# Kernel tuning notes

Measured on AMD Instinct MI355X. Metric: run time of the kernel, lower is better.

## Reference

```python
import jax, jax.numpy as jnp
import numpy as np

B, N, DIM, H, DH, MLP, L = 4, 1024, 1024, 16, 64, 4096, 2
C = DIM // 4  # conditioning dim = 256


def setup_inputs() -> dict:
    key = jax.random.key(0)
    ks = jax.random.split(key, 12)
    s = 0.02
    return dict(
        x=jax.random.normal(ks[0], (B, N, DIM), jnp.float32),
        mu=jax.random.normal(ks[1], (B, N, C), jnp.float32),
        f=jax.random.normal(ks[2], (B, N, C), jnp.float32),
        Wqkv=jax.random.normal(ks[3], (L, DIM, 3 * H * DH), jnp.float32) * s,
        Wout=jax.random.normal(ks[4], (L, H * DH, DIM), jnp.float32) * s,
        bout=jnp.zeros((L, DIM), jnp.float32),
        W1=jax.random.normal(ks[5], (L, DIM, MLP), jnp.float32) * s,
        b1=jnp.zeros((L, MLP), jnp.float32),
        W2=jax.random.normal(ks[6], (L, MLP, DIM), jnp.float32) * s,
        b2=jnp.zeros((L, DIM), jnp.float32),
        Wmu=jax.random.normal(ks[7], (L, C, 6 * C), jnp.float32) * s,
        bmu=jnp.zeros((L, 6 * C), jnp.float32),
        Wf=jax.random.normal(ks[8], (L, C, 6 * 3 * C), jnp.float32) * s,
        bf=jnp.zeros((L, 6 * 3 * C), jnp.float32),
        g1=jnp.ones((L, DIM), jnp.float32),
        be1=jnp.zeros((L, DIM), jnp.float32),
        g2=jnp.ones((L, DIM), jnp.float32),
        be2=jnp.zeros((L, DIM), jnp.float32),
    )


def _ln(x, g, b):
    m = jnp.mean(x, -1, keepdims=True)
    v = jnp.mean((x - m) ** 2, -1, keepdims=True)
    return (x - m) * jax.lax.rsqrt(v + 1e-5) * g + b


def reference(x, mu, f, Wqkv, Wout, bout, W1, b1, W2, b2, Wmu, bmu, Wf, bf, g1, be1, g2, be2):
    scale = DH ** -0.5
    smu = jax.nn.silu(mu)  # SiLU applied to raw conditioning, shared across layers
    sf = jax.nn.silu(f)
    for i in range(L):
        mm = smu @ Wmu[i] + bmu[i]          # [B,N,6*C]
        mf = sf @ Wf[i] + bf[i]             # [B,N,6*3*C]
        mus = jnp.split(mm, 6, axis=-1)     # each [B,N,C]
        fs = jnp.split(mf, 6, axis=-1)      # each [B,N,3C]
        sh_a, sc_a, ga_a, sh_m, sc_m, ga_m = [
            jnp.concatenate([a, b_], -1) for a, b_ in zip(mus, fs)
        ]                                   # each [B,N,DIM]
        # attention branch
        h = _ln(x, g1[i], be1[i]) * (1 + sc_a) + sh_a
        qkv = h @ Wqkv[i]                   # [B,N,3*H*DH]
        q, k, v = [t.reshape(B, N, H, DH) for t in jnp.split(qkv, 3, axis=-1)]
        att = jax.nn.softmax(jnp.einsum('bihd,bjhd->bhij', q, k) * scale, axis=-1)
        o = jnp.einsum('bhij,bjhd->bihd', att, v).reshape(B, N, H * DH)
        x = x + ga_a * (o @ Wout[i] + bout[i])
        # MLP branch
        h2 = _ln(x, g2[i], be2[i]) * (1 + sc_m) + sh_m
        mlp = jax.nn.gelu(h2 @ W1[i] + b1[i], approximate=False) @ W2[i] + b2[i]
        x = x + ga_m * mlp
    return x
```

## Files before the change

### kernel.cpp

```cpp
#include <hip/hip_runtime.h>
#include <math.h>

#define BB 4
#define NN 1024
#define DIMD 1024
#define HHN 16
#define DHH 64
#define MLPD 4096
#define LLN 2
#define CCD 256
#define BNROWS (BB*NN)

typedef __attribute__((ext_vector_type(8))) _Float16 h8;
typedef __attribute__((ext_vector_type(4))) _Float16 h4;
typedef __attribute__((ext_vector_type(4))) float f32x4;

#define GLD16(gp, lp) __builtin_amdgcn_global_load_lds( \
    (const __attribute__((address_space(1))) void*)(gp), \
    (__attribute__((address_space(3))) void*)(lp), 16, 0, 0)

__global__ __launch_bounds__(256) void silu_kernel(const float* __restrict__ in,
                                                   _Float16* __restrict__ out, int n4) {
  int i = blockIdx.x * 256 + threadIdx.x;
  if (i < n4) {
    float4 v = ((const float4*)in)[i];
    h4 o;
    o[0] = (_Float16)(v.x / (1.f + __expf(-v.x)));
    o[1] = (_Float16)(v.y / (1.f + __expf(-v.y)));
    o[2] = (_Float16)(v.z / (1.f + __expf(-v.z)));
    o[3] = (_Float16)(v.w / (1.f + __expf(-v.w)));
    ((h4*)out)[i] = o;
  }
}

__global__ __launch_bounds__(256) void transpose_cast(const float* __restrict__ in,
                                                      _Float16* __restrict__ out,
                                                      int K, int N) {
  __shared__ float tile[64][68];
  int bx = blockIdx.x * 64;
  int by = blockIdx.y * 64;
  int tid = threadIdx.x;
  int r0 = tid >> 4, c4 = (tid & 15) * 4;
  #pragma unroll
  for (int i = 0; i < 4; i++) {
    float4 v = *(const float4*)(in + (size_t)(by + r0 + i * 16) * N + bx + c4);
    *(float4*)&tile[r0 + i * 16][c4] = v;
  }
  __syncthreads();
  #pragma unroll
  for (int i = 0; i < 4; i++) {
    int orow = r0 + i * 16;
    h4 o;
    #pragma unroll
    for (int j = 0; j < 4; j++) o[j] = (_Float16)tile[c4 + j][orow];
    *(h4*)(out + (size_t)(bx + orow) * K + by + c4) = o;
  }
}

__global__ __launch_bounds__(256) void v_transpose(const _Float16* __restrict__ qkv,
                                                   _Float16* __restrict__ vt) {
  __shared__ _Float16 t[64][72];
  int n0 = blockIdx.x * 64;
  int bh = blockIdx.y;
  int b = bh >> 4;
  const _Float16* src = qkv + (size_t)b * NN * 3072 + 2048 + (bh & 15) * 64;
  int tid = threadIdx.x;
  int row = tid >> 2, c0 = (tid & 3) * 16;
  *(h8*)&t[row][c0] = *(const h8*)(src + (size_t)(n0 + row) * 3072 + c0);
  *(h8*)&t[row][c0 + 8] = *(const h8*)(src + (size_t)(n0 + row) * 3072 + c0 + 8);
  __syncthreads();
  int d = tid >> 2, ns = (tid & 3) * 16;
  h8 o0, o1;
  #pragma unroll
  for (int j = 0; j < 8; j++) { o0[j] = t[ns + j][d]; o1[j] = t[ns + 8 + j][d]; }
  _Float16* dst = vt + ((size_t)bh * 64 + d) * NN + n0 + ns;
  *(h8*)dst = o0;
  *(h8*)(dst + 8) = o1;
}

template <int EPI, int BNT>
__global__ __launch_bounds__(256) void gemm_bt(
    const _Float16* __restrict__ A, const _Float16* __restrict__ Bt,
    int M, int Nt, int K,
    const float* __restrict__ bias,
    _Float16* __restrict__ outh,
    float* __restrict__ xio,
    const _Float16* __restrict__ mmb, const _Float16* __restrict__ mfb, int gchunk) {
  constexpr int NREP = BNT / 32;
  __shared__ _Float16 As[3][128 * 32];
  __shared__ _Float16 Bs[3][BNT * 32];
  const int tid = threadIdx.x;
  const int wave = tid >> 6, lane = tid & 63;
  const int brow = blockIdx.x * 128, bcol = blockIdx.y * BNT;
  const int wr = (wave >> 1) * 64, wc = (wave & 1) * (BNT / 2);
  const int r = lane & 15, g = lane >> 4;
  f32x4 acc[4][NREP];
  #pragma unroll
  for (int m = 0; m < 4; m++)
    #pragma unroll
    for (int n = 0; n < NREP; n++) acc[m][n] = (f32x4){0.f, 0.f, 0.f, 0.f};

  const int scol = ((lane & 3) ^ ((lane >> 3) & 3)) * 8;
  const _Float16* gA = A + (size_t)(brow + wave * 32 + (lane >> 2)) * K + scol;
  const _Float16* gB = Bt + (size_t)(bcol + wave * (BNT / 4) + (lane >> 2)) * K + scol;

  auto STAGE = [&](int slot, int k0) {
    GLD16(gA + k0, &As[slot][wave * 1024]);
    GLD16(gA + k0 + 16 * (size_t)K, &As[slot][wave * 1024 + 512]);
    if (BNT == 128) {
      GLD16(gB + k0, &Bs[slot][wave * 1024]);
      GLD16(gB + k0 + 16 * (size_t)K, &Bs[slot][wave * 1024 + 512]);
    } else {
      GLD16(gB + k0, &Bs[slot][wave * 512]);
    }
  };

  const int NT = K / 32;
  #pragma unroll
  for (int s = 0; s < 3; ++s)
    if (s < NT) STAGE(s, s * 32);

  const int gg = g ^ ((r >> 1) & 3);

  int cur = 0;
  for (int t = 0; t < NT; ++t) {
    const int rem = NT - 1 - t;
    if constexpr (BNT == 128) {
      if (rem >= 2)      asm volatile("s_waitcnt vmcnt(8)" ::: "memory");
      else if (rem == 1) asm volatile("s_waitcnt vmcnt(4)" ::: "memory");
      else               asm volatile("s_waitcnt vmcnt(0)" ::: "memory");
    } else {
      if (rem >= 2)      asm volatile("s_waitcnt vmcnt(6)" ::: "memory");
      else if (rem == 1) asm volatile("s_waitcnt vmcnt(3)" ::: "memory");
      else               asm volatile("s_waitcnt vmcnt(0)" ::: "memory");
    }
    __builtin_amdgcn_s_barrier();
    h8 af[4], bfr[NREP];
    #pragma unroll
    for (int m = 0; m < 4; m++) af[m] = *(const h8*)(&As[cur][(wr + m * 16 + r) * 32 + gg * 8]);
    #pragma unroll
    for (int n = 0; n < NREP; n++) bfr[n] = *(const h8*)(&Bs[cur][(wc + n * 16 + r) * 32 + gg * 8]);
    #pragma unroll
    for (int m = 0; m < 4; m++)
      #pragma unroll
      for (int n = 0; n < NREP; n++)
        acc[m][n] = __builtin_amdgcn_mfma_f32_16x16x32_f16(bfr[n], af[m], acc[m][n], 0, 0, 0);
    asm volatile("s_waitcnt lgkmcnt(0)" ::: "memory");
    __builtin_amdgcn_s_barrier();
    if (t + 3 < NT) STAGE(cur, (t + 3) * 32);
    cur = (cur == 2) ? 0 : cur + 1;
  }

  #pragma unroll
  for (int m = 0; m < 4; m++) {
    const int grow = brow + wr + m * 16 + r;
    #pragma unroll
    for (int n = 0; n < NREP; n++) {
      const int gcol = bcol + wc + n * 16 + 4 * g;
      float4 bv4 = bias ? *(const float4*)(bias + gcol) : float4{0.f, 0.f, 0.f, 0.f};
      float v[4] = {acc[m][n][0] + bv4.x, acc[m][n][1] + bv4.y,
                    acc[m][n][2] + bv4.z, acc[m][n][3] + bv4.w};
      if (EPI == 0) {
        h4 o;
        #pragma unroll
        for (int q = 0; q < 4; q++) o[q] = (_Float16)v[q];
        *(h4*)(outh + (size_t)grow * Nt + gcol) = o;
      } else if (EPI == 1) {
        h4 o;
        #pragma unroll
        for (int q = 0; q < 4; q++)
          o[q] = (_Float16)(0.5f * v[q] * (1.f + erff(v[q] * 0.70710678118f)));
        *(h4*)(outh + (size_t)grow * Nt + gcol) = o;
      } else {
        h4 gav = (gcol < CCD)
            ? *(const h4*)(mmb + (size_t)grow * (6 * CCD) + gchunk * CCD + gcol)
            : *(const h4*)(mfb + (size_t)grow * (18 * CCD) + gchunk * (3 * CCD) + (gcol - CCD));
        float4 xv = *(float4*)(xio + (size_t)grow * DIMD + gcol);
        xv.x += (float)gav[0] * v[0];
        xv.y += (float)gav[1] * v[1];
        xv.z += (float)gav[2] * v[2];
        xv.w += (float)gav[3] * v[3];
        *(float4*)(xio + (size_t)grow * DIMD + gcol) = xv;
      }
    }
  }
}

__global__ __launch_bounds__(256) void ln_mod(const float* __restrict__ x,
                                              const float* __restrict__ gam,
                                              const float* __restrict__ bet,
                                              const _Float16* __restrict__ mmb,
                                              const _Float16* __restrict__ mfb,
                                              int jsh, int jsc,
                                              _Float16* __restrict__ hout) {
  const int row = blockIdx.x;
  const int tid = threadIdx.x;
  const float* xr = x + (size_t)row * DIMD;
  float4 v = ((const float4*)xr)[tid];
  float s = v.x + v.y + v.z + v.w;
  float sq = v.x * v.x + v.y * v.y + v.z * v.z + v.w * v.w;
  #pragma unroll
  for (int off = 32; off > 0; off >>= 1) {
    s += __shfl_down(s, off);
    sq += __shfl_down(sq, off);
  }
  __shared__ float red[8];
  int wv = tid >> 6, ln = tid & 63;
  if (ln == 0) { red[wv] = s; red[4 + wv] = sq; }
  __syncthreads();
  s = red[0] + red[1] + red[2] + red[3];
  sq = red[4] + red[5] + red[6] + red[7];
  float mean = s * (1.f / DIMD);
  float var = sq * (1.f / DIMD) - mean * mean;
  float rs = rsqrtf(var + 1e-5f);
  int c0 = tid * 4;
  float4 gm = ((const float4*)gam)[tid];
  float4 bt = ((const float4*)bet)[tid];
  float xv[4] = {v.x, v.y, v.z, v.w};
  float gv[4] = {gm.x, gm.y, gm.z, gm.w};
  float bv[4] = {bt.x, bt.y, bt.z, bt.w};
  h4 o;
  #pragma unroll
  for (int i = 0; i < 4; i++) {
    int c = c0 + i;
    float lnv = (xv[i] - mean) * rs * gv[i] + bv[i];
    float shv, scv;
    if (c < CCD) {
      shv = (float)mmb[(size_t)row * (6 * CCD) + jsh * CCD + c];
      scv = (float)mmb[(size_t)row * (6 * CCD) + jsc * CCD + c];
    } else {
      shv = (float)mfb[(size_t)row * (18 * CCD) + jsh * (3 * CCD) + (c - CCD)];
      scv = (float)mfb[(size_t)row * (18 * CCD) + jsc * (3 * CCD) + (c - CCD)];
    }
    o[i] = (_Float16)(lnv * (1.f + scv) + shv);
  }
  *((h4*)(hout + (size_t)row * DIMD + c0)) = o;
}

__global__ __launch_bounds__(256) void attn_kernel(const _Float16* __restrict__ qkv,
                                                   const _Float16* __restrict__ vt,
                                                   _Float16* __restrict__ o) {
  __shared__ _Float16 Ks[2 * 64 * 64];
  __shared__ _Float16 Vs[2 * 64 * 64];
  __shared__ _Float16 Ps[4][32 * 72];
  const int bhg = blockIdx.x * 8 + (blockIdx.y & 7);
  const int qt = blockIdx.y >> 3;
  const int b = bhg >> 4, hh = bhg & 15;
  const int tid = threadIdx.x;
  const int wave = tid >> 6, lane = tid & 63;
  const int r = lane & 15, g = lane >> 4;
  const int RS = 3 * HHN * DHH;
  const _Float16* qb = qkv + (size_t)b * NN * RS + hh * DHH;
  const _Float16* kb = qb + HHN * DHH;
  const _Float16* vtb = vt + (size_t)bhg * DHH * NN;
  const int q0 = qt * 128 + wave * 32;

  h8 qf[2][2];
  #pragma unroll
  for (int m = 0; m < 2; m++) {
    qf[m][0] = *(const h8*)(qb + (size_t)(q0 + m * 16 + r) * RS + g * 8);
    qf[m][1] = *(const h8*)(qb + (size_t)(q0 + m * 16 + r) * RS + 32 + g * 8);
  }

  f32x4 oacc[2][4];
  #pragma unroll
  for (int m = 0; m < 2; m++)
    #pragma unroll
    for (int n = 0; n < 4; n++) oacc[m][n] = (f32x4){0.f, 0.f, 0.f, 0.f};
  float mrun[2][4], lrun[2][4];
  #pragma unroll
  for (int m = 0; m < 2; m++)
    #pragma unroll
    for (int q = 0; q < 4; q++) { mrun[m][q] = -1e30f; lrun[m][q] = 0.f; }
  const float scale = 0.125f;
  _Float16* Pw = Ps[wave];

  auto STAGE = [&](int buf, int k0) {
    #pragma unroll
    for (int i = 0; i < 2; i++) {
      int chunk = wave * 2 + i;
      int blk = chunk * 64 + lane;
      int row = blk >> 3, c16 = blk & 7;
      int sc = ((c16 ^ (row & 7))) * 8;
      GLD16(kb + (size_t)(k0 + row) * RS + sc, Ks + buf * 4096 + chunk * 512);
      GLD16(vtb + (size_t)row * NN + k0 + sc, Vs + buf * 4096 + chunk * 512);
    }
  };

  STAGE(0, 0);
  int cur = 0;
  for (int kt = 0; kt < NN / 64; ++kt) {
    __syncthreads();
    if (kt + 1 < NN / 64) STAGE(cur ^ 1, (kt + 1) * 64);
    const _Float16* Kb = Ks + cur * 4096;
    const _Float16* Vb = Vs + cur * 4096;
    f32x4 sfr[2][4];
    #pragma unroll
    for (int m = 0; m < 2; m++)
      #pragma unroll
      for (int n = 0; n < 4; n++) sfr[m][n] = (f32x4){0.f, 0.f, 0.f, 0.f};
    #pragma unroll
    for (int n = 0; n < 4; n++) {
      int row = n * 16 + r, sw = row & 7;
      h8 kf0 = *(const h8*)(Kb + row * 64 + (g ^ sw) * 8);
      h8 kf1 = *(const h8*)(Kb + row * 64 + ((4 + g) ^ sw) * 8);
      #pragma unroll
      for (int m = 0; m < 2; m++) {
        sfr[m][n] = __builtin_amdgcn_mfma_f32_16x16x32_f16(qf[m][0], kf0, sfr[m][n], 0, 0, 0);
        sfr[m][n] = __builtin_amdgcn_mfma_f32_16x16x32_f16(qf[m][1], kf1, sfr[m][n], 0, 0, 0);
      }
    }
    #pragma unroll
    for (int m = 0; m < 2; m++) {
      float pm[4];
      #pragma unroll
      for (int q = 0; q < 4; q++)
        pm[q] = fmaxf(fmaxf(sfr[m][0][q], sfr[m][1][q]), fmaxf(sfr[m][2][q], sfr[m][3][q])) * scale;
      #pragma unroll
      for (int off = 1; off < 16; off <<= 1)
        #pragma unroll
        for (int q = 0; q < 4; q++) pm[q] = fmaxf(pm[q], __shfl_xor(pm[q], off));
      float fac[4], rsum[4];
      #pragma unroll
      for (int q = 0; q < 4; q++) {
        float mn = fmaxf(mrun[m][q], pm[q]);
        fac[q] = __expf(mrun[m][q] - mn);
        mrun[m][q] = mn;
        rsum[q] = 0.f;
      }
      #pragma unroll
      for (int n = 0; n < 4; n++)
        #pragma unroll
        for (int q = 0; q < 4; q++) {
          float p = __expf(sfr[m][n][q] * scale - mrun[m][q]);
          sfr[m][n][q] = p;
          rsum[q] += p;
        }
      #pragma unroll
      for (int off = 1; off < 16; off <<= 1)
        #pragma unroll
        for (int q = 0; q < 4; q++) rsum[q] += __shfl_xor(rsum[q], off);
      #pragma unroll
      for (int q = 0; q < 4; q++) lrun[m][q] = lrun[m][q] * fac[q] + rsum[q];
      #pragma unroll
      for (int n = 0; n < 4; n++)
        #pragma unroll
        for (int q = 0; q < 4; q++) oacc[m][n][q] *= fac[q];
      #pragma unroll
      for (int n = 0; n < 4; n++)
        #pragma unroll
        for (int q = 0; q < 4; q++)
          Pw[(m * 16 + 4 * g + q) * 72 + n * 16 + r] = (_Float16)sfr[m][n][q];
    }
    h8 pa[2][2];
    #pragma unroll
    for (int m = 0; m < 2; m++) {
      pa[m][0] = *(const h8*)(Pw + (m * 16 + r) * 72 + g * 8);
      pa[m][1] = *(const h8*)(Pw + (m * 16 + r) * 72 + 32 + g * 8);
    }
    #pragma unroll
    for (int nd = 0; nd < 4; nd++) {
      int row = nd * 16 + r, sw = row & 7;
      h8 vf0 = *(const h8*)(Vb + row * 64 + (g ^ sw) * 8);
      h8 vf1 = *(const h8*)(Vb + row * 64 + ((4 + g) ^ sw) * 8);
      #pragma unroll
      for (int m = 0; m < 2; m++) {
        oacc[m][nd] = __builtin_amdgcn_mfma_f32_16x16x32_f16(pa[m][0], vf0, oacc[m][nd], 0, 0, 0);
        oacc[m][nd] = __builtin_amdgcn_mfma_f32_16x16x32_f16(pa[m][1], vf1, oacc[m][nd], 0, 0, 0);
      }
    }
    cur ^= 1;
  }
  #pragma unroll
  for (int m = 0; m < 2; m++)
    #pragma unroll
    for (int nd = 0; nd < 4; nd++)
      #pragma unroll
      for (int q = 0; q < 4; q++) {
        int row = q0 + m * 16 + 4 * g + q;
        int col = hh * DHH + nd * 16 + r;
        o[((size_t)b * NN + row) * DIMD + col] = (_Float16)(oacc[m][nd][q] / lrun[m][q]);
      }
}

extern "C" void kernel_launch(void* const* d_in, const int* in_sizes, int n_in,
                              void* d_out, int out_size, void* d_ws, size_t ws_size,
                              hipStream_t stream) {
  (void)in_sizes; (void)n_in; (void)out_size; (void)ws_size;
  const float* mu   = (const float*)d_in[1];
  const float* f_in = (const float*)d_in[2];
  const float* Wqkv = (const float*)d_in[3];
  const float* Wout = (const float*)d_in[4];
  const float* bout = (const float*)d_in[5];
  const float* W1   = (const float*)d_in[6];
  const float* b1   = (const float*)d_in[7];
  const float* W2   = (const float*)d_in[8];
  const float* b2   = (const float*)d_in[9];
  const float* Wmu  = (const float*)d_in[10];
  const float* bmu  = (const float*)d_in[11];
  const float* Wf   = (const float*)d_in[12];
  const float* bfv  = (const float*)d_in[13];
  const float* g1   = (const float*)d_in[14];
  const float* be1  = (const float*)d_in[15];
  const float* g2   = (const float*)d_in[16];
  const float* be2  = (const float*)d_in[17];
  float* xout = (float*)d_out;

  char* ws = (char*)d_ws;
  size_t off = 0;
  auto alloc = [&](size_t elems) -> _Float16* {
    _Float16* p = (_Float16*)(ws + off);
    off += ((elems * 2 + 255) / 256) * 256;
    return p;
  };
  _Float16* wTqkv = alloc((size_t)LLN * 3072 * 1024);
  _Float16* wTout = alloc((size_t)LLN * 1024 * 1024);
  _Float16* wT1   = alloc((size_t)LLN * 4096 * 1024);
  _Float16* wT2   = alloc((size_t)LLN * 1024 * 4096);
  _Float16* wTmu  = alloc((size_t)LLN * 1536 * 256);
  _Float16* wTf   = alloc((size_t)LLN * 4608 * 256);
  _Float16* smu   = alloc((size_t)BNROWS * CCD);
  _Float16* sfb   = alloc((size_t)BNROWS * CCD);
  _Float16* mmb   = alloc((size_t)BNROWS * 6 * CCD);
  _Float16* mfb   = alloc((size_t)BNROWS * 18 * CCD);
  _Float16* hbuf  = alloc((size_t)BNROWS * DIMD);
  _Float16* qkvb  = alloc((size_t)BNROWS * 3 * DIMD);
  _Float16* obuf  = alloc((size_t)BNROWS * DIMD);
  _Float16* m1b   = alloc((size_t)BNROWS * MLPD);
  _Float16* vtb   = alloc((size_t)BNROWS * DIMD);

  hipMemcpyAsync(d_out, d_in[0], (size_t)BNROWS * DIMD * sizeof(float),
                 hipMemcpyDeviceToDevice, stream);

  silu_kernel<<<BNROWS * CCD / 4 / 256, 256, 0, stream>>>(mu, smu, BNROWS * CCD / 4);
  silu_kernel<<<BNROWS * CCD / 4 / 256, 256, 0, stream>>>(f_in, sfb, BNROWS * CCD / 4);

  for (int l = 0; l < LLN; l++) {
    transpose_cast<<<dim3(3072 / 64, 1024 / 64), 256, 0, stream>>>(
        Wqkv + (size_t)l * 1024 * 3072, wTqkv + (size_t)l * 3072 * 1024, 1024, 3072);
    transpose_cast<<<dim3(1024 / 64, 1024 / 64), 256, 0, stream>>>(
        Wout + (size_t)l * 1024 * 1024, wTout + (size_t)l * 1024 * 1024, 1024, 1024);
    transpose_cast<<<dim3(4096 / 64, 1024 / 64), 256, 0, stream>>>(
        W1 + (size_t)l * 1024 * 4096, wT1 + (size_t)l * 4096 * 1024, 1024, 4096);
    transpose_cast<<<dim3(1024 / 64, 4096 / 64), 256, 0, stream>>>(
        W2 + (size_t)l * 4096 * 1024, wT2 + (size_t)l * 1024 * 4096, 4096, 1024);
    transpose_cast<<<dim3(1536 / 64, 256 / 64), 256, 0, stream>>>(
        Wmu + (size_t)l * 256 * 1536, wTmu + (size_t)l * 1536 * 256, 256, 1536);
    transpose_cast<<<dim3(4608 / 64, 256 / 64), 256, 0, stream>>>(
        Wf + (size_t)l * 256 * 4608, wTf + (size_t)l * 4608 * 256, 256, 4608);
  }

  for (int l = 0; l < LLN; l++) {
    gemm_bt<0, 64><<<dim3(BNROWS / 128, 1536 / 64), 256, 0, stream>>>(
        smu, wTmu + (size_t)l * 1536 * 256, BNROWS, 1536, 256,
        bmu + (size_t)l * 1536, mmb, nullptr, nullptr, nullptr, 0);
    gemm_bt<0, 128><<<dim3(BNROWS / 128, 4608 / 128), 256, 0, stream>>>(
        sfb, wTf + (size_t)l * 4608 * 256, BNROWS, 4608, 256,
        bfv + (size_t)l * 4608, mfb, nullptr, nullptr, nullptr, 0);
    ln_mod<<<BNROWS, 256, 0, stream>>>(xout, g1 + (size_t)l * DIMD, be1 + (size_t)l * DIMD,
                                       mmb, mfb, 0, 1, hbuf);
    gemm_bt<0, 128><<<dim3(BNROWS / 128, 3072 / 128), 256, 0, stream>>>(
        hbuf, wTqkv + (size_t)l * 3072 * 1024, BNROWS, 3072, 1024,
        nullptr, qkvb, nullptr, nullptr, nullptr, 0);
    v_transpose<<<dim3(NN / 64, BB * HHN), 256, 0, stream>>>(qkvb, vtb);
    attn_kernel<<<dim3(NN / 128, BB * HHN), 256, 0, stream>>>(qkvb, vtb, obuf);
    gemm_bt<2, 64><<<dim3(BNROWS / 128, 1024 / 64), 256, 0, stream>>>(
        obuf, wTout + (size_t)l * 1024 * 1024, BNROWS, 1024, 1024,
        bout + (size_t)l * DIMD, nullptr, xout, mmb, mfb, 2);
    ln_mod<<<BNROWS, 256, 0, stream>>>(xout, g2 + (size_t)l * DIMD, be2 + (size_t)l * DIMD,
                                       mmb, mfb, 3, 4, hbuf);
    gemm_bt<1, 128><<<dim3(BNROWS / 128, 4096 / 128), 256, 0, stream>>>(
        hbuf, wT1 + (size_t)l * 4096 * 1024, BNROWS, 4096, 1024,
        b1 + (size_t)l * MLPD, m1b, nullptr, nullptr, nullptr, 0);
    gemm_bt<2, 64><<<dim3(BNROWS / 128, 1024 / 64), 256, 0, stream>>>(
        m1b, wT2 + (size_t)l * 1024 * 4096, BNROWS, 1024, 4096,
        b2 + (size_t)l * DIMD, nullptr, xout, mmb, mfb, 5);
  }
}
```

Before: 703.9 us.

## Move gated residual add from GEMM epilogue into LayerNorm-modulation kernel

The out-projection and second MLP GEMMs now write an fp16 delta buffer instead of doing a read-modify-write of the fp32 residual with gate loads in their epilogue. The gated residual add is folded into the following LayerNorm/modulation kernel, with a final residual kernel after the last layer, and the modulation buffers are double-buffered per layer so the previous layer's gate remains available. The LN kernel also switches to vectorized h4 loads for shift and scale. This simplifies the GEMM epilogues but adds an fp16 delta round trip and rounds the branch output to fp16 before it is added to the residual.

```diff
diff --git a/kernel.cpp b/kernel.cpp
--- a/kernel.cpp
+++ b/kernel.cpp
@@ -83,9 +83,7 @@
     const _Float16* __restrict__ A, const _Float16* __restrict__ Bt,
     int M, int Nt, int K,
     const float* __restrict__ bias,
-    _Float16* __restrict__ outh,
-    float* __restrict__ xio,
-    const _Float16* __restrict__ mmb, const _Float16* __restrict__ mfb, int gchunk) {
+    _Float16* __restrict__ outh) {
   constexpr int NREP = BNT / 32;
   __shared__ _Float16 As[3][128 * 32];
   __shared__ _Float16 Bs[3][BNT * 32];
@@ -160,43 +158,43 @@
       float4 bv4 = bias ? *(const float4*)(bias + gcol) : float4{0.f, 0.f, 0.f, 0.f};
       float v[4] = {acc[m][n][0] + bv4.x, acc[m][n][1] + bv4.y,
                     acc[m][n][2] + bv4.z, acc[m][n][3] + bv4.w};
+      h4 o;
       if (EPI == 0) {
-        h4 o;
         #pragma unroll
         for (int q = 0; q < 4; q++) o[q] = (_Float16)v[q];
-        *(h4*)(outh + (size_t)grow * Nt + gcol) = o;
-      } else if (EPI == 1) {
-        h4 o;
+      } else {
         #pragma unroll
         for (int q = 0; q < 4; q++)
           o[q] = (_Float16)(0.5f * v[q] * (1.f + erff(v[q] * 0.70710678118f)));
-        *(h4*)(outh + (size_t)grow * Nt + gcol) = o;
-      } else {
-        h4 gav = (gcol < CCD)
-            ? *(const h4*)(mmb + (size_t)grow * (6 * CCD) + gchunk * CCD + gcol)
-            : *(const h4*)(mfb + (size_t)grow * (18 * CCD) + gchunk * (3 * CCD) + (gcol - CCD));
-        float4 xv = *(float4*)(xio + (size_t)grow * DIMD + gcol);
-        xv.x += (float)gav[0] * v[0];
-        xv.y += (float)gav[1] * v[1];
-        xv.z += (float)gav[2] * v[2];
-        xv.w += (float)gav[3] * v[3];
-        *(float4*)(xio + (size_t)grow * DIMD + gcol) = xv;
       }
-    }
-  }
-}
-
-__global__ __launch_bounds__(256) void ln_mod(const float* __restrict__ x,
-                                              const float* __restrict__ gam,
-                                              const float* __restrict__ bet,
-                                              const _Float16* __restrict__ mmb,
-                                              const _Float16* __restrict__ mfb,
-                                              int jsh, int jsc,
-                                              _Float16* __restrict__ hout) {
+      *(h4*)(outh + (size_t)grow * Nt + gcol) = o;
+    }
+  }
+}
+
+__global__ __launch_bounds__(256) void ln_mod_res(
+    float* __restrict__ x,
+    const _Float16* __restrict__ delta,
+    const _Float16* __restrict__ mga, const _Float16* __restrict__ fga, int jga,
+    const _Float16* __restrict__ msc, const _Float16* __restrict__ fsc, int jsh, int jsc,
+    const float* __restrict__ gam, const float* __restrict__ bet,
+    _Float16* __restrict__ hout) {
   const int row = blockIdx.x;
   const int tid = threadIdx.x;
-  const float* xr = x + (size_t)row * DIMD;
-  float4 v = ((const float4*)xr)[tid];
+  const int c0 = tid * 4;
+  float* xr = x + (size_t)row * DIMD;
+  float4 v = *(float4*)(xr + c0);
+  if (delta) {
+    h4 d4 = *(const h4*)(delta + (size_t)row * DIMD + c0);
+    h4 g4 = (c0 < CCD)
+        ? *(const h4*)(mga + (size_t)row * (6 * CCD) + jga * CCD + c0)
+        : *(const h4*)(fga + (size_t)row * (18 * CCD) + jga * (3 * CCD) + (c0 - CCD));
+    v.x += (float)g4[0] * (float)d4[0];
+    v.y += (float)g4[1] * (float)d4[1];
+    v.z += (float)g4[2] * (float)d4[2];
+    v.w += (float)g4[3] * (float)d4[3];
+    *(float4*)(xr + c0) = v;
+  }
   float s = v.x + v.y + v.z + v.w;
   float sq = v.x * v.x + v.y * v.y + v.z * v.z + v.w * v.w;
   #pragma unroll
@@ -213,28 +211,42 @@
   float mean = s * (1.f / DIMD);
   float var = sq * (1.f / DIMD) - mean * mean;
   float rs = rsqrtf(var + 1e-5f);
-  int c0 = tid * 4;
-  float4 gm = ((const float4*)gam)[tid];
-  float4 bt = ((const float4*)bet)[tid];
+  float4 gm = *(const float4*)(gam + c0);
+  float4 bt = *(const float4*)(bet + c0);
+  h4 sh4 = (c0 < CCD)
+      ? *(const h4*)(msc + (size_t)row * (6 * CCD) + jsh * CCD + c0)
+      : *(const h4*)(fsc + (size_t)row * (18 * CCD) + jsh * (3 * CCD) + (c0 - CCD));
+  h4 sc4 = (c0 < CCD)
+      ? *(const h4*)(msc + (size_t)row * (6 * CCD) + jsc * CCD + c0)
+      : *(const h4*)(fsc + (size_t)row * (18 * CCD) + jsc * (3 * CCD) + (c0 - CCD));
   float xv[4] = {v.x, v.y, v.z, v.w};
   float gv[4] = {gm.x, gm.y, gm.z, gm.w};
   float bv[4] = {bt.x, bt.y, bt.z, bt.w};
   h4 o;
   #pragma unroll
   for (int i = 0; i < 4; i++) {
-    int c = c0 + i;
     float lnv = (xv[i] - mean) * rs * gv[i] + bv[i];
-    float shv, scv;
-    if (c < CCD) {
-      shv = (float)mmb[(size_t)row * (6 * CCD) + jsh * CCD + c];
-      scv = (float)mmb[(size_t)row * (6 * CCD) + jsc * CCD + c];
-    } else {
-      shv = (float)mfb[(size_t)row * (18 * CCD) + jsh * (3 * CCD) + (c - CCD)];
-      scv = (float)mfb[(size_t)row * (18 * CCD) + jsc * (3 * CCD) + (c - CCD)];
-    }
-    o[i] = (_Float16)(lnv * (1.f + scv) + shv);
+    o[i] = (_Float16)(lnv * (1.f + (float)sc4[i]) + (float)sh4[i]);
   }
   *((h4*)(hout + (size_t)row * DIMD + c0)) = o;
+}
+
+__global__ __launch_bounds__(256) void res_final(
+    float* __restrict__ x, const _Float16* __restrict__ delta,
+    const _Float16* __restrict__ mga, const _Float16* __restrict__ fga, int jga) {
+  const int row = blockIdx.x;
+  const int c0 = threadIdx.x * 4;
+  float* xr = x + (size_t)row * DIMD;
+  float4 v = *(float4*)(xr + c0);
+  h4 d4 = *(const h4*)(delta + (size_t)row * DIMD + c0);
+  h4 g4 = (c0 < CCD)
+      ? *(const h4*)(mga + (size_t)row * (6 * CCD) + jga * CCD + c0)
+      : *(const h4*)(fga + (size_t)row * (18 * CCD) + jga * (3 * CCD) + (c0 - CCD));
+  v.x += (float)g4[0] * (float)d4[0];
+  v.y += (float)g4[1] * (float)d4[1];
+  v.z += (float)g4[2] * (float)d4[2];
+  v.w += (float)g4[3] * (float)d4[3];
+  *(float4*)(xr + c0) = v;
 }
 
 __global__ __launch_bounds__(256) void attn_kernel(const _Float16* __restrict__ qkv,
@@ -421,13 +433,14 @@
   _Float16* wTf   = alloc((size_t)LLN * 4608 * 256);
   _Float16* smu   = alloc((size_t)BNROWS * CCD);
   _Float16* sfb   = alloc((size_t)BNROWS * CCD);
-  _Float16* mmb   = alloc((size_t)BNROWS * 6 * CCD);
-  _Float16* mfb   = alloc((size_t)BNROWS * 18 * CCD);
+  _Float16* mmb[2] = {alloc((size_t)BNROWS * 6 * CCD), alloc((size_t)BNROWS * 6 * CCD)};
+  _Float16* mfb[2] = {alloc((size_t)BNROWS * 18 * CCD), alloc((size_t)BNROWS * 18 * CCD)};
   _Float16* hbuf  = alloc((size_t)BNROWS * DIMD);
   _Float16* qkvb  = alloc((size_t)BNROWS * 3 * DIMD);
   _Float16* obuf  = alloc((size_t)BNROWS * DIMD);
   _Float16* m1b   = alloc((size_t)BNROWS * MLPD);
   _Float16* vtb   = alloc((size_t)BNROWS * DIMD);
+  _Float16* dres  = alloc((size_t)BNROWS * DIMD);
 
   hipMemcpyAsync(d_out, d_in[0], (size_t)BNROWS * DIMD * sizeof(float),
                  hipMemcpyDeviceToDevice, stream);
@@ -453,27 +466,34 @@
   for (int l = 0; l < LLN; l++) {
     gemm_bt<0, 64><<<dim3(BNROWS / 128, 1536 / 64), 256, 0, stream>>>(
         smu, wTmu + (size_t)l * 1536 * 256, BNROWS, 1536, 256,
-        bmu + (size_t)l * 1536, mmb, nullptr, nullptr, nullptr, 0);
+        bmu + (size_t)l * 1536, mmb[l]);
     gemm_bt<0, 128><<<dim3(BNROWS / 128, 4608 / 128), 256, 0, stream>>>(
         sfb, wTf + (size_t)l * 4608 * 256, BNROWS, 4608, 256,
-        bfv + (size_t)l * 4608, mfb, nullptr, nullptr, nullptr, 0);
-    ln_mod<<<BNROWS, 256, 0, stream>>>(xout, g1 + (size_t)l * DIMD, be1 + (size_t)l * DIMD,
-                                       mmb, mfb, 0, 1, hbuf);
+        bfv + (size_t)l * 4608, mfb[l]);
+    ln_mod_res<<<BNROWS, 256, 0, stream>>>(
+        xout, (l == 0) ? nullptr : dres,
+        mmb[l ^ 1], mfb[l ^ 1], 5,
+        mmb[l], mfb[l], 0, 1,
+        g1 + (size_t)l * DIMD, be1 + (size_t)l * DIMD, hbuf);
     gemm_bt<0, 128><<<dim3(BNROWS / 128, 3072 / 128), 256, 0, stream>>>(
         hbuf, wTqkv + (size_t)l * 3072 * 1024, BNROWS, 3072, 1024,
-        nullptr, qkvb, nullptr, nullptr, nullptr, 0);
+        nullptr, qkvb);
     v_transpose<<<dim3(NN / 64, BB * HHN), 256, 0, stream>>>(qkvb, vtb);
     attn_kernel<<<dim3(NN / 128, BB * HHN), 256, 0, stream>>>(qkvb, vtb, obuf);
-    gemm_bt<2, 64><<<dim3(BNROWS / 128, 1024 / 64), 256, 0, stream>>>(
+    gemm_bt<0, 64><<<dim3(BNROWS / 128, 1024 / 64), 256, 0, stream>>>(
         obuf, wTout + (size_t)l * 1024 * 1024, BNROWS, 1024, 1024,
-        bout + (size_t)l * DIMD, nullptr, xout, mmb, mfb, 2);
-    ln_mod<<<BNROWS, 256, 0, stream>>>(xout, g2 + (size_t)l * DIMD, be2 + (size_t)l * DIMD,
-                                       mmb, mfb, 3, 4, hbuf);
+        bout + (size_t)l * DIMD, dres);
+    ln_mod_res<<<BNROWS, 256, 0, stream>>>(
+        xout, dres,
+        mmb[l], mfb[l], 2,
+        mmb[l], mfb[l], 3, 4,
+        g2 + (size_t)l * DIMD, be2 + (size_t)l * DIMD, hbuf);
     gemm_bt<1, 128><<<dim3(BNROWS / 128, 4096 / 128), 256, 0, stream>>>(
         hbuf, wT1 + (size_t)l * 4096 * 1024, BNROWS, 4096, 1024,
-        b1 + (size_t)l * MLPD, m1b, nullptr, nullptr, nullptr, 0);
-    gemm_bt<2, 64><<<dim3(BNROWS / 128, 1024 / 64), 256, 0, stream>>>(
+        b1 + (size_t)l * MLPD, m1b);
+    gemm_bt<0, 64><<<dim3(BNROWS / 128, 1024 / 64), 256, 0, stream>>>(
         m1b, wT2 + (size_t)l * 1024 * 4096, BNROWS, 1024, 4096,
-        b2 + (size_t)l * DIMD, nullptr, xout, mmb, mfb, 5);
-  }
-}
+        b2 + (size_t)l * DIMD, dres);
+  }
+  res_final<<<BNROWS, 256, 0, stream>>>(xout, dres, mmb[(LLN - 1) & 1], mfb[(LLN - 1) & 1], 5);
+}
```

Measured after the change: 724.1 us. 1.03x slower.
